# Performance work log

Hardware: AMD Instinct MI355X
Metric: run time of the kernel (lower is better)

The kernel has to match this reference:

```python
import jax, jax.numpy as jnp
import numpy as np

H = 4  # fixed number of heads in the layer


def setup_inputs() -> dict:
    key = jax.random.key(0)
    ks = jax.random.split(key, 6)
    B, S, D = 4, 2048, 512
    U = 2 * D  # per-head projection width (units = d_model * 2)
    x = jax.random.normal(ks[0], (B, S, D), dtype=jnp.float32)
    gamma = jnp.ones((D,), dtype=jnp.float32)
    beta = jnp.zeros((D,), dtype=jnp.float32)
    s = 0.02
    Wq = jax.random.normal(ks[1], (H, D, U), dtype=jnp.float32) * s
    Wk = jax.random.normal(ks[2], (H, D, U), dtype=jnp.float32) * s
    Wv = jax.random.normal(ks[3], (H, D, U), dtype=jnp.float32) * s
    Wout = jax.random.normal(ks[4], (H * U, D), dtype=jnp.float32) * s
    return {"x": x, "gamma": gamma, "beta": beta, "Wq": Wq, "Wk": Wk, "Wv": Wv, "Wout": Wout}


def _forward(x, gamma, beta, Wq, Wk, Wv, Wout):
    B, S, D = x.shape
    eps = 1e-6
    # LayerNormalization over last axis (Keras default, eps=1e-6)
    mu = jnp.mean(x, axis=-1, keepdims=True)
    var = jnp.mean(jnp.square(x - mu), axis=-1, keepdims=True)
    xn = (x - mu) * jax.lax.rsqrt(var + eps) * gamma + beta
    # Per-head Q/K/V projections, batched over head axis. Dropout is identity at inference.
    q = jnp.einsum('bsd,hdu->bhsu', xn, Wq)
    k = jnp.einsum('bsd,hdu->bhsu', xn, Wk)
    v = jnp.einsum('bsd,hdu->bhsu', xn, Wv)
    # Keras Attention(use_scale=False, causal=True): unscaled dot-product scores
    scores = jnp.einsum('bhsu,bhtu->bhst', q, k)  # [B,H,S,S]
    causal = jnp.tril(jnp.ones((S, S), dtype=bool))
    scores = jnp.where(causal, scores, jnp.finfo(scores.dtype).min)
    probs = jax.nn.softmax(scores, axis=-1)
    head = jnp.einsum('bhst,bhtu->bhsu', probs, v)  # [B,H,S,U]
    # concat heads in head order -> [B,S,H*U], then output Dense back to D
    HU = head.shape[1] * head.shape[3]
    cat = head.transpose(0, 2, 1, 3).reshape(B, S, HU)
    return cat @ Wout


def reference(x, gamma, beta, Wq, Wk, Wv, Wout):
    return _forward(x, gamma, beta, Wq, Wk, Wv, Wout)
```

## Files before the change

kernel.cpp:

```cpp
#include <hip/hip_runtime.h>

typedef _Float16 half8 __attribute__((ext_vector_type(8)));
typedef float floatx4 __attribute__((ext_vector_type(4)));

__device__ __forceinline__ void gl16(const _Float16* g, _Float16* l) {
    __builtin_amdgcn_global_load_lds((const __attribute__((address_space(1))) void*)g,
                                     (__attribute__((address_space(3))) void*)l, 16, 0, 0);
}

#define Scst 2048
#define Dcst 512
#define Ucst 1024
#define Hcst 4
#define SDo 1048576LL
#define UDo 524288LL
#define SUo 2097152LL
#define SSo 4194304LL
#define USo 2097152LL
#define SHUo 8388608LL

__global__ __launch_bounds__(64) void ln_k(const float* __restrict__ x,
                                           const float* __restrict__ gamma,
                                           const float* __restrict__ beta,
                                           _Float16* __restrict__ xn) {
    const int D = 512;
    long long base = (long long)blockIdx.x * D;
    int lane = threadIdx.x;
    floatx4 x0 = *(const floatx4*)(x + base + lane * 8);
    floatx4 x1 = *(const floatx4*)(x + base + lane * 8 + 4);
    float f[8];
#pragma unroll
    for (int i = 0; i < 4; i++) { f[i] = x0[i]; f[4 + i] = x1[i]; }
    float s = 0.f, ss = 0.f;
#pragma unroll
    for (int i = 0; i < 8; i++) { s += f[i]; ss += f[i] * f[i]; }
#pragma unroll
    for (int off = 32; off; off >>= 1) { s += __shfl_xor(s, off); ss += __shfl_xor(ss, off); }
    float mean = s * (1.f / 512.f);
    float var = ss * (1.f / 512.f) - mean * mean;
    float rstd = rsqrtf(var + 1e-6f);
    floatx4 g0 = *(const floatx4*)(gamma + lane * 8);
    floatx4 g1 = *(const floatx4*)(gamma + lane * 8 + 4);
    floatx4 b0 = *(const floatx4*)(beta + lane * 8);
    floatx4 b1 = *(const floatx4*)(beta + lane * 8 + 4);
    half8 o;
#pragma unroll
    for (int i = 0; i < 4; i++) {
        o[i]     = (_Float16)((f[i]     - mean) * rstd * g0[i] + b0[i]);
        o[4 + i] = (_Float16)((f[4 + i] - mean) * rstd * g1[i] + b1[i]);
    }
    *(half8*)(xn + base + lane * 8) = o;
}

__global__ __launch_bounds__(256) void tr_k(const float* __restrict__ in,
                                            _Float16* __restrict__ out, int R, int C) {
    __shared__ _Float16 tile[32][33];
    int tx = threadIdx.x, ty = threadIdx.y;
    long long zo = (long long)blockIdx.z * R * C;
    int r0 = blockIdx.y * 32, c0 = blockIdx.x * 32;
    for (int yy = ty; yy < 32; yy += 8)
        tile[yy][tx] = (_Float16)in[zo + (long long)(r0 + yy) * C + c0 + tx];
    __syncthreads();
    for (int yy = ty; yy < 32; yy += 8)
        out[zo + (long long)(c0 + yy) * R + r0 + tx] = tile[tx][yy];
}

#define BM 128
#define BN 128
#define BK 32
__global__ __launch_bounds__(256) void gemm_bt(
    const _Float16* __restrict__ A, const _Float16* __restrict__ Bt, void* __restrict__ Cv,
    int K, int ldc, int cflags, int mode, int ldab) {
    int z = blockIdx.z;
    long long offA = 0, offB = 0, offC = 0;
    switch (mode) {
        case 6:
            offB = (long long)(z & 7) * UDo; offC = (long long)z * SUo;
            break;
        case 7:
            offA = (long long)(z & 3) * UDo; offC = (long long)z * USo;
            break;
        case 8:
            offA = (long long)z * 1024; offB = (long long)z * 1024;
            offC = (long long)z * SUo;
            break;
        default: break;
    }
    const _Float16* Ab = A + offA;
    const _Float16* Bb = Bt + offB;

    int gx = gridDim.x, gy = gridDim.y;
    int nb = gx * gy;
    int lin = blockIdx.y * gx + blockIdx.x;
    int mIdx, nIdx;
    if (((nb & 7) == 0) && ((gx & 3) == 0)) {
        int chunk = nb >> 3;
        int vid = (lin >> 3) + chunk * (lin & 7);
        int panelH = gy * 4;
        int panel = vid / panelH;
        int rem = vid - panel * panelH;
        mIdx = rem >> 2;
        nIdx = (panel << 2) + (rem & 3);
    } else { mIdx = blockIdx.y; nIdx = blockIdx.x; }
    int m0 = mIdx * BM, n0 = nIdx * BN;

    if ((cflags & 4) && n0 > m0 + (BM - 1)) return;
    int kend = (cflags & 8) ? min(K, m0 + BM) : K;

    __shared__ _Float16 As[2][BM * BK];
    __shared__ _Float16 Bs[2][BN * BK];

    int t = threadIdx.x;
    int srow = t >> 2;
    int scol = (t & 3) * 8;
    int lane = t & 63, w = t >> 6;
    int wm = (w >> 1) * 64, wn = (w & 1) * 64;
    int lm = lane & 15, lk = (lane >> 4) * 8;

    floatx4 acc[4][4];
#pragma unroll
    for (int i = 0; i < 4; i++)
#pragma unroll
        for (int j = 0; j < 4; j++) acc[i][j] = floatx4{0.f, 0.f, 0.f, 0.f};

    const _Float16* ga0 = Ab + (long long)(m0 + srow) * ldab + scol;
    const _Float16* ga1 = Ab + (long long)(m0 + 64 + srow) * ldab + scol;
    const _Float16* gb0 = Bb + (long long)(n0 + srow) * ldab + scol;
    const _Float16* gb1 = Bb + (long long)(n0 + 64 + srow) * ldab + scol;

    int nIter = kend / BK;
    gl16(ga0, &As[0][t * 8]);
    gl16(ga1, &As[0][2048 + t * 8]);
    gl16(gb0, &Bs[0][t * 8]);
    gl16(gb1, &Bs[0][2048 + t * 8]);

    for (int it = 0; it < nIter; it++) {
        __syncthreads();
        int cur = it & 1;
        half8 af[4], bfr[4];
#pragma unroll
        for (int i = 0; i < 4; i++) af[i] = *(const half8*)&As[cur][(wm + i * 16 + lm) * BK + lk];
#pragma unroll
        for (int j = 0; j < 4; j++) bfr[j] = *(const half8*)&Bs[cur][(wn + j * 16 + lm) * BK + lk];
        if (it + 1 < nIter) {
            int nk = (it + 1) * BK;
            int nxt = cur ^ 1;
            gl16(ga0 + nk, &As[nxt][t * 8]);
            gl16(ga1 + nk, &As[nxt][2048 + t * 8]);
            gl16(gb0 + nk, &Bs[nxt][t * 8]);
            gl16(gb1 + nk, &Bs[nxt][2048 + t * 8]);
        }
#pragma unroll
        for (int i = 0; i < 4; i++)
#pragma unroll
            for (int j = 0; j < 4; j++)
                acc[i][j] = __builtin_amdgcn_mfma_f32_16x16x32_f16(af[i], bfr[j], acc[i][j], 0, 0, 0);
    }

    int cr = (lane >> 4) * 4;
    int cc = lm;
    bool outf32 = (cflags & 1) != 0;
#pragma unroll
    for (int i = 0; i < 4; i++) {
#pragma unroll
        for (int j = 0; j < 4; j++) {
            int rr = m0 + wm + i * 16 + cr;
            int nn = n0 + wn + j * 16 + cc;
#pragma unroll
            for (int r2 = 0; r2 < 4; r2++) {
                long long idx = (long long)(rr + r2) * ldc + nn + offC;
                float val = acc[i][j][r2];
                if (outf32) ((float*)Cv)[idx] = val;
                else ((_Float16*)Cv)[idx] = (_Float16)val;
            }
        }
    }
}

__global__ __launch_bounds__(256) void redk(const float* __restrict__ part,
                                            float* __restrict__ o, int n4) {
    long long stride = (long long)gridDim.x * 256;
    for (long long i = blockIdx.x * 256 + threadIdx.x; i < n4; i += stride) {
        floatx4 s = *(const floatx4*)(part + i * 4);
#pragma unroll
        for (int c = 1; c < 4; c++) {
            floatx4 v = *(const floatx4*)(part + (long long)c * n4 * 4 + i * 4);
            s[0] += v[0]; s[1] += v[1]; s[2] += v[2]; s[3] += v[3];
        }
        *(floatx4*)(o + i * 4) = s;
    }
}

__global__ __launch_bounds__(512, 2) void gemm_bt256(
    const _Float16* __restrict__ A, const _Float16* __restrict__ Bt, void* __restrict__ Cv,
    int K, int ldc, int cflags, int mode) {
    int z = blockIdx.z;
    long long offA = 0, offB = 0, offC = 0;
    switch (mode) {
        case 1:
            offA = (long long)((z >> 2) & 1) * SDo;
            offB = (long long)(((z >> 3) * 4) + (z & 3)) * UDo;
            offC = (long long)(((z >> 3) * 8) + ((z & 3) * 2) + ((z >> 2) & 1)) * SUo;
            break;
        case 2:
            offA = (long long)z * SUo; offB = (long long)z * SUo; offC = (long long)z * SSo;
            break;
        case 3:
            offA = (long long)(z >> 1) * UDo; offB = (long long)(z & 1) * SDo;
            offC = (long long)z * USo;
            break;
        case 4:
            offA = (long long)z * SSo; offB = (long long)z * USo;
            offC = (long long)(z & 1) * SHUo + (long long)(z >> 1) * Ucst;
            break;
        default: break;
    }
    const _Float16* Ab = A + offA;
    const _Float16* Bb = Bt + offB;

    int gx = gridDim.x;
    int nwg = gx * gridDim.y;
    int lin = blockIdx.y * gx + blockIdx.x;
    int q8 = nwg >> 3, r8 = nwg & 7;
    int xcd = lin & 7, sub8 = lin >> 3;
    int wg = (xcd < r8 ? xcd * (q8 + 1) : r8 * (q8 + 1) + (xcd - r8) * q8) + sub8;
    int m0 = (wg / gx) * 256, n0 = (wg % gx) * 256;

    if ((cflags & 4) && n0 > m0 + 255) return;
    int kend = (cflags & 8) ? min(K, m0 + 256) : K;
    int NT = kend >> 6;

    __shared__ _Float16 SH[65536];
#define ASX(b, k, i) SH[((b) << 14) + ((k) << 13) + (i)]
#define BSX(b, k, i) SH[32768 + ((b) << 14) + ((k) << 13) + (i)]

    int t = threadIdx.x;
    int lane = t & 63, w = t >> 6;
    int wm = (w >> 2) * 128, wn = (w & 3) * 64;
    int lm = lane & 15, ls = lane >> 4;
    int sw8 = ((ls ^ ((lm >> 1) & 3)) << 3);

    long long stoff = (long long)(t >> 2) * K + (((t & 3) ^ ((t >> 3) & 3)) << 3);
    const _Float16* gA = Ab + (long long)m0 * K + stoff;
    const _Float16* gB = Bb + (long long)n0 * K + stoff;
    long long rowK = 128LL * K;
    int ldd = t * 8;

    floatx4 acc[8][4];
#pragma unroll
    for (int i = 0; i < 8; i++)
#pragma unroll
        for (int j = 0; j < 4; j++) acc[i][j] = floatx4{0.f, 0.f, 0.f, 0.f};

#define STGA(v, ks) { const _Float16* s_ = gA + (((v) << 6) + ((ks) << 5)); \
        gl16(s_, &ASX((v) & 1, ks, ldd)); gl16(s_ + rowK, &ASX((v) & 1, ks, 4096 + ldd)); }
#define STGB(v, ks) { const _Float16* s_ = gB + (((v) << 6) + ((ks) << 5)); \
        gl16(s_, &BSX((v) & 1, ks, ldd)); gl16(s_ + rowK, &BSX((v) & 1, ks, 4096 + ldd)); }
#define RDA(mm, ks) (*(const half8*)&ASX(cur, ks, (wm + (mm) * 16 + lm) * 32 + sw8))
#define RDB(nn, ks) (*(const half8*)&BSX(cur, ks, (wn + (nn) * 16 + lm) * 32 + sw8))
#define MFMA32() \
    _Pragma("unroll") for (int mm = 0; mm < 8; mm++) \
    _Pragma("unroll") for (int nn = 0; nn < 4; nn++) \
        acc[mm][nn] = __builtin_amdgcn_mfma_f32_16x16x32_f16( \
            af[mm], bf[nn], acc[mm][nn], 0, 0, 0);

    STGA(0, 0) STGB(0, 0) STGA(0, 1) STGB(0, 1) STGA(1, 0) STGB(1, 0)
    asm volatile("s_waitcnt vmcnt(8)" ::: "memory");
    __builtin_amdgcn_s_barrier();

    for (int tt = 0; tt < NT; tt++) {
        int cur = tt & 1;
        bool more = (tt + 1 < NT);
        {
            half8 af[8], bf[4];
            bf[0] = RDB(0, 0); bf[1] = RDB(1, 0); bf[2] = RDB(2, 0); bf[3] = RDB(3, 0);
            af[0] = RDA(0, 0); af[1] = RDA(1, 0); af[2] = RDA(2, 0); af[3] = RDA(3, 0);
            af[4] = RDA(4, 0); af[5] = RDA(5, 0); af[6] = RDA(6, 0); af[7] = RDA(7, 0);
            if (more) asm volatile("s_waitcnt vmcnt(4)" ::: "memory");
            else      asm volatile("s_waitcnt vmcnt(0)" ::: "memory");
            __builtin_amdgcn_s_barrier();
            if (more) { STGA(tt + 1, 1) STGB(tt + 1, 1) }
            __builtin_amdgcn_s_setprio(1);
            MFMA32()
            __builtin_amdgcn_s_setprio(0);
        }
        {
            half8 af[8], bf[4];
            bf[0] = RDB(0, 1); bf[1] = RDB(1, 1); bf[2] = RDB(2, 1); bf[3] = RDB(3, 1);
            af[0] = RDA(0, 1); af[1] = RDA(1, 1); af[2] = RDA(2, 1); af[3] = RDA(3, 1);
            af[4] = RDA(4, 1); af[5] = RDA(5, 1); af[6] = RDA(6, 1); af[7] = RDA(7, 1);
            if (more) asm volatile("s_waitcnt vmcnt(4)" ::: "memory");
            else      asm volatile("s_waitcnt vmcnt(0)" ::: "memory");
            __builtin_amdgcn_s_barrier();
            if (tt + 2 < NT) { STGA(tt + 2, 0) STGB(tt + 2, 0) }
            __builtin_amdgcn_s_setprio(1);
            MFMA32()
            __builtin_amdgcn_s_setprio(0);
        }
    }

    __builtin_amdgcn_s_barrier();
    int cr = ls * 4;
#pragma unroll
    for (int i = 0; i < 8; i++) {
#pragma unroll
        for (int j = 0; j < 4; j++) {
#pragma unroll
            for (int r2 = 0; r2 < 4; r2++) {
                int row = wm + i * 16 + cr + r2;
                int col = wn + j * 16 + lm;
                SH[row * 256 + (col ^ ((row & 3) << 3))] = (_Float16)acc[i][j][r2];
            }
        }
    }
    __builtin_amdgcn_s_barrier();
    _Float16* Ch = (_Float16*)Cv;
    int cchunk = t & 31;
    int rbase = t >> 5;
#pragma unroll
    for (int it = 0; it < 16; it++) {
        int r = rbase + it * 16;
        half8 v = *(const half8*)&SH[r * 256 + ((cchunk ^ (r & 3)) << 3)];
        *(half8*)&Ch[(long long)(m0 + r) * ldc + n0 + (cchunk << 3) + offC] = v;
    }
#undef STGA
#undef STGB
#undef RDA
#undef RDB
#undef MFMA32
#undef ASX
#undef BSX
}

__global__ __launch_bounds__(256) void softmax_h(_Float16* __restrict__ sc, int S) {
    int wid = threadIdx.x >> 6, lane = threadIdx.x & 63;
    int idx = blockIdx.x * 4 + wid;
    int r = idx & (S - 1);
    _Float16* srow = sc + (long long)idx * S;
    int nc = r >> 9;
    float v[32];
    float mx = -3.0e38f;
    for (int c = 0; c <= nc; c++) {
        half8 hv = *(half8*)(srow + lane * 8 + c * 512);
#pragma unroll
        for (int i = 0; i < 8; i++) {
            int n = lane * 8 + c * 512 + i;
            float s = (n <= r) ? (float)hv[i] : -3.0e38f;
            v[c * 8 + i] = s; mx = fmaxf(mx, s);
        }
    }
#pragma unroll
    for (int off = 32; off; off >>= 1) mx = fmaxf(mx, __shfl_xor(mx, off));
    float sum = 0.f;
    for (int c = 0; c <= nc; c++)
#pragma unroll
        for (int i = 0; i < 8; i++) {
            int n = lane * 8 + c * 512 + i;
            float e = (n <= r) ? __expf(v[c * 8 + i] - mx) : 0.f;
            v[c * 8 + i] = e; sum += e;
        }
#pragma unroll
    for (int off = 32; off; off >>= 1) sum += __shfl_xor(sum, off);
    float inv = 1.f / sum;
    for (int c = 0; c <= nc; c++) {
        half8 o;
#pragma unroll
        for (int i = 0; i < 8; i++) o[i] = (_Float16)(v[c * 8 + i] * inv);
        *(half8*)(srow + lane * 8 + c * 512) = o;
    }
}

extern "C" void kernel_launch(void* const* d_in, const int* in_sizes, int n_in,
                              void* d_out, int out_size, void* d_ws, size_t ws_size,
                              hipStream_t stream) {
    const int B = 4, S = 2048, D = 512, H = 4, U = 1024;
    const float* x     = (const float*)d_in[0];
    const float* gamma = (const float*)d_in[1];
    const float* beta  = (const float*)d_in[2];
    const float* Wq    = (const float*)d_in[3];
    const float* Wk    = (const float*)d_in[4];
    const float* Wv    = (const float*)d_in[5];
    const float* Wout  = (const float*)d_in[6];
    float* out = (float*)d_out;

    char* ws = (char*)d_ws;
    const size_t MiB = 1ull << 20;
    const long long SD = SDo, UD = UDo, SU = SUo, US = USo;

    _Float16* xn  = (_Float16*)(ws + 0);
    _Float16* WqT = (_Float16*)(ws + 8  * MiB);
    _Float16* WkT = (_Float16*)(ws + 12 * MiB);
    _Float16* WvT = (_Float16*)(ws + 16 * MiB);
    _Float16* WoT = (_Float16*)(ws + 20 * MiB);

    tr_k<<<dim3(U / 32, D / 32, H), dim3(32, 8), 0, stream>>>(Wq, WqT, D, U);
    tr_k<<<dim3(U / 32, D / 32, H), dim3(32, 8), 0, stream>>>(Wk, WkT, D, U);
    tr_k<<<dim3(U / 32, D / 32, H), dim3(32, 8), 0, stream>>>(Wv, WvT, D, U);
    tr_k<<<dim3(D / 32, (H * U) / 32, 1), dim3(32, 8), 0, stream>>>(Wout, WoT, H * U, D);
    ln_k<<<B * S, 64, 0, stream>>>(x, gamma, beta, xn);

    if (ws_size >= 168 * MiB) {
        _Float16* qk  = (_Float16*)(ws + 24 * MiB);
        _Float16* kk  = qk + 8 * SU;
        _Float16* sc  = (_Float16*)(ws + 88 * MiB);
        _Float16* vt  = qk;
        _Float16* cat = kk;
        float* part   = (float*)(ws + 88 * MiB);

        for (int p = 0; p < 2; p++) {
            const _Float16* xnp = xn + (long long)p * 2 * SD;
            float* outp = out + (long long)p * 2 * SD;
            gemm_bt256<<<dim3(U / 256, S / 256, 16), 512, 0, stream>>>(xnp, WqT, qk, D, U, 0, 1);
            gemm_bt256<<<dim3(S / 256, S / 256, 8), 512, 0, stream>>>(qk, kk, sc, U, S, 4, 2);
            softmax_h<<<8 * S / 4, 256, 0, stream>>>(sc, S);
            gemm_bt256<<<dim3(S / 256, U / 256, 8), 512, 0, stream>>>(WvT, xnp, vt, D, S, 0, 3);
            gemm_bt256<<<dim3(U / 256, S / 256, 8), 512, 0, stream>>>(sc, vt, cat, S, H * U, 8, 4);
            gemm_bt<<<dim3(D / 128, 2 * S / 128, 4), 256, 0, stream>>>(cat, WoT, part,
                1024, D, 1, 8, H * U);
            redk<<<1024, 256, 0, stream>>>(part, outp, (int)(2 * SD / 4));
        }
    } else {
        _Float16* qb   = (_Float16*)(ws + 24 * MiB);
        _Float16* vTb  = (_Float16*)(ws + 56 * MiB);
        _Float16* catb = (_Float16*)(ws + 72 * MiB);
        _Float16* sc   = (_Float16*)(ws + 88 * MiB);

        for (int b = 0; b < B; b++) {
            const _Float16* xnb = xn + (long long)b * SD;
            gemm_bt<<<dim3(U / 128, S / 128, 2 * H), 256, 0, stream>>>(xnb, WqT, qb, D, U, 0, 6, D);
            gemm_bt<<<dim3(S / 128, U / 128, H), 256, 0, stream>>>(WvT, xnb, vTb, D, S, 0, 7, D);
            for (int h = 0; h < H; h++) {
                gemm_bt<<<dim3(S / 128, S / 128, 1), 256, 0, stream>>>(qb + (long long)h * SU,
                    qb + (long long)(H + h) * SU, sc, U, S, 4, 0, U);
                softmax_h<<<S / 4, 256, 0, stream>>>(sc, S);
                gemm_bt<<<dim3(U / 128, S / 128, 1), 256, 0, stream>>>(sc,
                    vTb + (long long)h * US, (void*)(catb + (long long)h * U), S, H * U, 8, 0, S);
            }
            gemm_bt<<<dim3(D / 128, S / 128, 1), 256, 0, stream>>>(catb, WoT,
                (void*)(out + (long long)b * SD), H * U, D, 1, 0, H * U);
        }
    }
}
```

Before: 606.3 us.

## Restructure GEMM main loop to whole-K-tile double buffering with 64-wide LDS rows

Replaces the split-k half-tile staging (two 32-wide k-slices per buffer with staggered prefetch and partial vmcnt waits) with a simpler scheme. Each iteration now prefetches a full 64-wide K tile into the other buffer, runs both MFMA halves, then waits for all loads and syncs once. LDS rows become 64 halves wide with an 8-way XOR swizzle. This cuts barriers per tile from two to one and simplifies the address math, but it waits on vmcnt(0) every iteration, which may expose more global-load latency than the staggered version did.

```diff
diff --git a/kernel.cpp b/kernel.cpp
--- a/kernel.cpp
+++ b/kernel.cpp
@@ -231,19 +231,20 @@
     int NT = kend >> 6;
 
     __shared__ _Float16 SH[65536];
-#define ASX(b, k, i) SH[((b) << 14) + ((k) << 13) + (i)]
-#define BSX(b, k, i) SH[32768 + ((b) << 14) + ((k) << 13) + (i)]
+#define ASX(b, i) SH[((b) << 14) + (i)]
+#define BSX(b, i) SH[32768 + ((b) << 14) + (i)]
 
     int t = threadIdx.x;
     int lane = t & 63, w = t >> 6;
     int wm = (w >> 2) * 128, wn = (w & 3) * 64;
     int lm = lane & 15, ls = lane >> 4;
-    int sw8 = ((ls ^ ((lm >> 1) & 3)) << 3);
-
-    long long stoff = (long long)(t >> 2) * K + (((t & 3) ^ ((t >> 3) & 3)) << 3);
+    int sl0 = ((ls ^ (lm >> 1)) << 3);
+    int sl1 = sl0 ^ 32;
+
+    long long stoff = (long long)(t >> 3) * K + (((t & 7) ^ ((t >> 4) & 7)) << 3);
     const _Float16* gA = Ab + (long long)m0 * K + stoff;
     const _Float16* gB = Bb + (long long)n0 * K + stoff;
-    long long rowK = 128LL * K;
+    long long rowK64 = 64LL * K;
     int ldd = t * 8;
 
     floatx4 acc[8][4];
@@ -252,54 +253,41 @@
 #pragma unroll
         for (int j = 0; j < 4; j++) acc[i][j] = floatx4{0.f, 0.f, 0.f, 0.f};
 
-#define STGA(v, ks) { const _Float16* s_ = gA + (((v) << 6) + ((ks) << 5)); \
-        gl16(s_, &ASX((v) & 1, ks, ldd)); gl16(s_ + rowK, &ASX((v) & 1, ks, 4096 + ldd)); }
-#define STGB(v, ks) { const _Float16* s_ = gB + (((v) << 6) + ((ks) << 5)); \
-        gl16(s_, &BSX((v) & 1, ks, ldd)); gl16(s_ + rowK, &BSX((v) & 1, ks, 4096 + ldd)); }
-#define RDA(mm, ks) (*(const half8*)&ASX(cur, ks, (wm + (mm) * 16 + lm) * 32 + sw8))
-#define RDB(nn, ks) (*(const half8*)&BSX(cur, ks, (wn + (nn) * 16 + lm) * 32 + sw8))
-#define MFMA32() \
-    _Pragma("unroll") for (int mm = 0; mm < 8; mm++) \
-    _Pragma("unroll") for (int nn = 0; nn < 4; nn++) \
-        acc[mm][nn] = __builtin_amdgcn_mfma_f32_16x16x32_f16( \
-            af[mm], bf[nn], acc[mm][nn], 0, 0, 0);
-
-    STGA(0, 0) STGB(0, 0) STGA(0, 1) STGB(0, 1) STGA(1, 0) STGB(1, 0)
-    asm volatile("s_waitcnt vmcnt(8)" ::: "memory");
+#define STG(v) { int b_ = (v) & 1; long long ko_ = ((long long)(v)) << 6; \
+        gl16(gA + ko_,               &ASX(b_, ldd)); \
+        gl16(gA + ko_ + rowK64,      &ASX(b_, 4096 + ldd)); \
+        gl16(gA + ko_ + 2 * rowK64,  &ASX(b_, 8192 + ldd)); \
+        gl16(gA + ko_ + 3 * rowK64,  &ASX(b_, 12288 + ldd)); \
+        gl16(gB + ko_,               &BSX(b_, ldd)); \
+        gl16(gB + ko_ + rowK64,      &BSX(b_, 4096 + ldd)); \
+        gl16(gB + ko_ + 2 * rowK64,  &BSX(b_, 8192 + ldd)); \
+        gl16(gB + ko_ + 3 * rowK64,  &BSX(b_, 12288 + ldd)); }
+#define RDA(mm, sl) (*(const half8*)&ASX(cur, (wm + (mm) * 16 + lm) * 64 + (sl)))
+#define RDB(nn, sl) (*(const half8*)&BSX(cur, (wn + (nn) * 16 + lm) * 64 + (sl)))
+#define MFMA32(sl) { half8 af[8], bf[4]; \
+      bf[0] = RDB(0, sl); bf[1] = RDB(1, sl); bf[2] = RDB(2, sl); bf[3] = RDB(3, sl); \
+      af[0] = RDA(0, sl); af[1] = RDA(1, sl); af[2] = RDA(2, sl); af[3] = RDA(3, sl); \
+      af[4] = RDA(4, sl); af[5] = RDA(5, sl); af[6] = RDA(6, sl); af[7] = RDA(7, sl); \
+      __builtin_amdgcn_s_setprio(1); \
+      _Pragma("unroll") for (int mm = 0; mm < 8; mm++) \
+      _Pragma("unroll") for (int nn = 0; nn < 4; nn++) \
+          acc[mm][nn] = __builtin_amdgcn_mfma_f32_16x16x32_f16( \
+              af[mm], bf[nn], acc[mm][nn], 0, 0, 0); \
+      __builtin_amdgcn_s_setprio(0); }
+
+    STG(0)
+    asm volatile("s_waitcnt vmcnt(0)" ::: "memory");
     __builtin_amdgcn_s_barrier();
 
     for (int tt = 0; tt < NT; tt++) {
         int cur = tt & 1;
-        bool more = (tt + 1 < NT);
-        {
-            half8 af[8], bf[4];
-            bf[0] = RDB(0, 0); bf[1] = RDB(1, 0); bf[2] = RDB(2, 0); bf[3] = RDB(3, 0);
-            af[0] = RDA(0, 0); af[1] = RDA(1, 0); af[2] = RDA(2, 0); af[3] = RDA(3, 0);
-            af[4] = RDA(4, 0); af[5] = RDA(5, 0); af[6] = RDA(6, 0); af[7] = RDA(7, 0);
-            if (more) asm volatile("s_waitcnt vmcnt(4)" ::: "memory");
-            else      asm volatile("s_waitcnt vmcnt(0)" ::: "memory");
-            __builtin_amdgcn_s_barrier();
-            if (more) { STGA(tt + 1, 1) STGB(tt + 1, 1) }
-            __builtin_amdgcn_s_setprio(1);
-            MFMA32()
-            __builtin_amdgcn_s_setprio(0);
-        }
-        {
-            half8 af[8], bf[4];
-            bf[0] = RDB(0, 1); bf[1] = RDB(1, 1); bf[2] = RDB(2, 1); bf[3] = RDB(3, 1);
-            af[0] = RDA(0, 1); af[1] = RDA(1, 1); af[2] = RDA(2, 1); af[3] = RDA(3, 1);
-            af[4] = RDA(4, 1); af[5] = RDA(5, 1); af[6] = RDA(6, 1); af[7] = RDA(7, 1);
-            if (more) asm volatile("s_waitcnt vmcnt(4)" ::: "memory");
-            else      asm volatile("s_waitcnt vmcnt(0)" ::: "memory");
-            __builtin_amdgcn_s_barrier();
-            if (tt + 2 < NT) { STGA(tt + 2, 0) STGB(tt + 2, 0) }
-            __builtin_amdgcn_s_setprio(1);
-            MFMA32()
-            __builtin_amdgcn_s_setprio(0);
-        }
-    }
-
-    __builtin_amdgcn_s_barrier();
+        if (tt + 1 < NT) STG(tt + 1)
+        MFMA32(sl0)
+        MFMA32(sl1)
+        asm volatile("s_waitcnt vmcnt(0)" ::: "memory");
+        __builtin_amdgcn_s_barrier();
+    }
+
     int cr = ls * 4;
 #pragma unroll
     for (int i = 0; i < 8; i++) {
@@ -323,8 +311,7 @@
         half8 v = *(const half8*)&SH[r * 256 + ((cchunk ^ (r & 3)) << 3)];
         *(half8*)&Ch[(long long)(m0 + r) * ldc + n0 + (cchunk << 3) + offC] = v;
     }
-#undef STGA
-#undef STGB
+#undef STG
 #undef RDA
 #undef RDB
 #undef MFMA32
```

After: 609.9 us. About the same (+0.6%).
